# Kernel tuning notes

Measured on AMD Instinct MI355X. Metric: run time of the kernel, lower is better.

The kernel has to match this reference:

```python
import jax, jax.numpy as jnp
import numpy as np

N, E, D_IN, HID, OUT, H = 50000, 800000, 64, 128, 128, 8


def _lin(key, fan_in, fan_out, bias=True):
    k1, k2 = jax.random.split(key)
    W = jax.random.normal(k1, (fan_in, fan_out), jnp.float32) / np.sqrt(fan_in)
    if bias:
        b = jax.random.normal(k2, (fan_out,), jnp.float32) * 0.01
        return W, b
    return (W,)


def setup_inputs() -> dict:
    key = jax.random.key(0)
    ks = jax.random.split(key, 40)
    inp = {
        "x": jax.random.normal(ks[0], (N, D_IN), jnp.float32),
        "edge_index": jax.random.randint(ks[1], (2, E), 0, N, jnp.int64),
        "edge_attr": jax.random.normal(ks[2], (E, D_IN), jnp.float32),
    }
    dims = [(D_IN, HID), (HID, HID), (HID, OUT)]  # (in, heads*out_ch) per layer
    ki = 3
    for l, (di, do) in enumerate(dims):
        inp[f"Wq{l}"], inp[f"bq{l}"] = _lin(ks[ki], di, do); ki += 1
        inp[f"Wk{l}"], inp[f"bk{l}"] = _lin(ks[ki], di, do); ki += 1
        inp[f"Wv{l}"], inp[f"bv{l}"] = _lin(ks[ki], di, do); ki += 1
        (inp[f"We{l}"],) = _lin(ks[ki], D_IN, do, bias=False); ki += 1
        inp[f"Ws{l}"], inp[f"bs{l}"] = _lin(ks[ki], di, do); ki += 1
    for l in range(2):
        inp[f"g{l}"] = jnp.ones((HID,), jnp.float32)
        inp[f"be{l}"] = jnp.zeros((HID,), jnp.float32)
    return inp


def _transformer_conv(x, src, dst, edge_attr, Wq, bq, Wk, bk, Wv, bv, We, Ws, bs):
    n = x.shape[0]
    hc = Wq.shape[1]
    c = hc // H
    q = (x @ Wq + bq).reshape(n, H, c)
    k = (x @ Wk + bk).reshape(n, H, c)
    v = (x @ Wv + bv).reshape(n, H, c)
    e = (edge_attr @ We).reshape(-1, H, c)  # [E,H,c]
    ke = k[src] + e                          # edge-wise key + edge proj
    alpha = jnp.einsum("ehc,ehc->eh", q[dst], ke) / jnp.sqrt(jnp.float32(c))
    m = jax.ops.segment_max(alpha, dst, num_segments=n)
    m = jnp.where(jnp.isfinite(m), m, 0.0)
    p = jnp.exp(alpha - m[dst])
    s = jax.ops.segment_sum(p, dst, num_segments=n)
    a = p / (s[dst] + 1e-16)                 # segment softmax over in-edges
    msg = (v[src] + e) * a[..., None]
    out = jax.ops.segment_sum(msg, dst, num_segments=n).reshape(n, hc)
    return out + x @ Ws + bs                 # root/skip connection


def _bn(x, g, b):
    mu = jnp.mean(x, axis=0)
    var = jnp.mean(jnp.square(x - mu), axis=0)
    return g * (x - mu) * jax.lax.rsqrt(var + 1e-5) + b


def reference(x, edge_index, edge_attr,
              Wq0, bq0, Wk0, bk0, Wv0, bv0, We0, Ws0, bs0,
              Wq1, bq1, Wk1, bk1, Wv1, bv1, We1, Ws1, bs1,
              Wq2, bq2, Wk2, bk2, Wv2, bv2, We2, Ws2, bs2,
              g0, be0, g1, be1):
    src, dst = edge_index[0], edge_index[1]
    h = _transformer_conv(x, src, dst, edge_attr, Wq0, bq0, Wk0, bk0, Wv0, bv0, We0, Ws0, bs0)
    h = jax.nn.relu(_bn(h, g0, be0))
    h = _transformer_conv(h, src, dst, edge_attr, Wq1, bq1, Wk1, bk1, Wv1, bv1, We1, Ws1, bs1)
    h = jax.nn.relu(_bn(h, g1, be1))
    h = _transformer_conv(h, src, dst, edge_attr, Wq2, bq2, Wk2, bk2, Wv2, bv2, We2, Ws2, bs2)
    return h, edge_attr
```

## Files before the change

### kernel.cpp

```cpp
#include <hip/hip_runtime.h>
#include <hip/hip_bf16.h>

typedef __attribute__((ext_vector_type(8))) short short8;
typedef __attribute__((ext_vector_type(4))) float f32x4;
typedef unsigned short ushort_t;
typedef __attribute__((ext_vector_type(2))) unsigned short ushort2v;
typedef __attribute__((ext_vector_type(2))) unsigned int uint2v;
typedef __attribute__((ext_vector_type(4))) unsigned int uint4v;

static __device__ __forceinline__ ushort_t f2bf(float x) {
    __hip_bfloat16 h = __float2bfloat16(x);
    return *(ushort_t*)&h;
}
static __device__ __forceinline__ float bflo(unsigned int u) { return __uint_as_float(u << 16); }
static __device__ __forceinline__ float bfhi(unsigned int u) { return __uint_as_float(u & 0xffff0000u); }
static __device__ __forceinline__ float bfu(ushort_t u) { return __uint_as_float((unsigned int)u << 16); }

template <int CTRL>
static __device__ __forceinline__ float dpp_xadd(float x) {
    int y = __builtin_amdgcn_update_dpp(0, __float_as_int(x), CTRL, 0xF, 0xF, true);
    return x + __int_as_float(y);
}
static __device__ __forceinline__ float swz4_add(float x) {
    int y = __builtin_amdgcn_ds_swizzle(__float_as_int(x), 0x101F);
    return x + __int_as_float(y);
}


__global__ void hist_kernel(const int* __restrict__ dst, int E, int* __restrict__ hist) {
    int i = blockIdx.x * blockDim.x + threadIdx.x;
    if (i < E) atomicAdd(&hist[dst[i]], 1);
}

__global__ __launch_bounds__(1024) void scan_block_kernel(
    const int* __restrict__ hist, int n, int* __restrict__ row_ptr, int* __restrict__ bsums)
{
    __shared__ int lds[1024];
    int tid = threadIdx.x;
    int i = blockIdx.x * 1024 + tid;
    int vv = (i < n) ? hist[i] : 0;
    lds[tid] = vv;
    __syncthreads();
    for (int off = 1; off < 1024; off <<= 1) {
        int t = (tid >= off) ? lds[tid - off] : 0;
        __syncthreads();
        lds[tid] += t;
        __syncthreads();
    }
    if (i < n) row_ptr[i] = lds[tid] - vv;
    if (tid == 1023) bsums[blockIdx.x] = lds[1023];
}

__global__ void scan_tops_kernel(int* __restrict__ bsums, int nb) {
    if (threadIdx.x == 0 && blockIdx.x == 0) {
        int run = 0;
        for (int i = 0; i < nb; i++) { int t = bsums[i]; bsums[i] = run; run += t; }
    }
}

__global__ __launch_bounds__(256) void scan_add_kernel(
    const int* __restrict__ bsums, int n, int total,
    int* __restrict__ row_ptr, int* __restrict__ cursor)
{
    int i = blockIdx.x * blockDim.x + threadIdx.x;
    if (i < n) {
        int vv = row_ptr[i] + bsums[i >> 10];
        row_ptr[i] = vv;
        cursor[i] = vv;
    }
    if (i == 0) row_ptr[n] = total;
}

__global__ void scatter_kernel(const int* __restrict__ src, const int* __restrict__ dst, int E,
                               int* __restrict__ cursor, int* __restrict__ inv, int* __restrict__ srcs) {
    int i = blockIdx.x * blockDim.x + threadIdx.x;
    if (i < E) {
        int d = dst[i];
        int pos = atomicAdd(&cursor[d], 1);
        inv[i] = pos;
        srcs[pos] = src[i];
    }
}

__global__ __launch_bounds__(256) void copy_permute_kernel(
    const float* __restrict__ edge_attr, const int* __restrict__ inv, int E,
    float* __restrict__ out_pass, ushort_t* __restrict__ ea)
{
    int idx = blockIdx.x * blockDim.x + threadIdx.x;
    if (idx >= E * 8) return;
    int i = idx >> 3, seg = idx & 7;
    const float* s = edge_attr + (size_t)i * 64 + seg * 8;
    float4 f0 = *(const float4*)s;
    float4 f1 = *(const float4*)(s + 4);
    float* d = out_pass + (size_t)i * 64 + seg * 8;
    *(float4*)d = f0;
    *(float4*)(d + 4) = f1;
    short8 o;
    o[0] = f2bf(f0.x); o[1] = f2bf(f0.y); o[2] = f2bf(f0.z); o[3] = f2bf(f0.w);
    o[4] = f2bf(f1.x); o[5] = f2bf(f1.y); o[6] = f2bf(f1.z); o[7] = f2bf(f1.w);
    int pos = inv[i];
    *(short8*)(ea + (size_t)pos * 64 + seg * 8) = o;
}

struct PackArgs {
    const float* We[3];
    const float* Wn[3][4];
    const float* bb[3][4];
};

__global__ __launch_bounds__(256) void pack_all_kernel(
    PackArgs pa, ushort_t* __restrict__ BpackE, ushort_t* __restrict__ BpackN,
    float* __restrict__ biasc)
{
    int idx = blockIdx.x * blockDim.x + threadIdx.x;
    if (idx < 24576) {
        int j = idx & 7, lane = (idx >> 3) & 63, kk = (idx >> 9) & 1,
            t = (idx >> 10) & 7, layer = idx >> 13;
        int kdim = kk * 32 + (lane >> 4) * 8 + j;
        int ncol = t * 16 + (lane & 15);
        BpackE[idx] = f2bf(pa.We[layer][kdim * 128 + ncol]);
    } else if (idx < 188416) {
        int local = idx - 24576;
        int layer, DI;
        if (local < 32768) { layer = 0; DI = 64; }
        else if (local < 98304) { layer = 1; DI = 128; local -= 32768; }
        else { layer = 2; DI = 128; local -= 98304; }
        int NKF = DI >> 5;
        int j = local & 7, lane = (local >> 3) & 63;
        int rest = local >> 9;
        int kf = rest % NKF, t = rest / NKF;
        int kdim = kf * 32 + (lane >> 4) * 8 + j;
        int ncol = t * 16 + (lane & 15);
        BpackN[layer * 65536 + local] = f2bf(pa.Wn[layer][ncol >> 7][kdim * 128 + (ncol & 127)]);
    } else if (idx < 189952) {
        int local = idx - 188416;
        int layer = local >> 9, i = local & 511;
        biasc[layer * 512 + i] = pa.bb[layer][i >> 7][i & 127];
    }
}

template <int DI, bool BN>
__global__ __launch_bounds__(256) void node_gemm_mfma_kernel(
    const float* __restrict__ hin, int N,
    const ushort_t* __restrict__ Bpack, const float* __restrict__ biasc,
    const float* __restrict__ scale, const float* __restrict__ shift,
    float* __restrict__ qout, unsigned int* __restrict__ kvout,
    float* __restrict__ skipout)
{
    constexpr int NKF = DI / 32;
    __shared__ float ctile[64][132];
    __shared__ ushort_t ctileK[64][136];
    int wave = threadIdx.x >> 6;
    int lane = threadIdx.x & 63;
    int tid = threadIdx.x;
    int base = blockIdx.x * 64;
    int m0 = base + wave * 16;

    int mrow = min(m0 + (lane & 15), N - 1);
    const float* arow = hin + (size_t)mrow * DI;
    int koff = (lane >> 4) * 8;

    short8 a[NKF];
#pragma unroll
    for (int kf = 0; kf < NKF; kf++) {
        float4 fa = *(const float4*)(arow + kf * 32 + koff);
        float4 fb = *(const float4*)(arow + kf * 32 + koff + 4);
        if constexpr (BN) {
            int c0 = kf * 32 + koff;
            float4 sa = *(const float4*)(scale + c0);
            float4 sb = *(const float4*)(scale + c0 + 4);
            float4 ha = *(const float4*)(shift + c0);
            float4 hb = *(const float4*)(shift + c0 + 4);
            fa.x = fmaxf(fa.x * sa.x + ha.x, 0.f);
            fa.y = fmaxf(fa.y * sa.y + ha.y, 0.f);
            fa.z = fmaxf(fa.z * sa.z + ha.z, 0.f);
            fa.w = fmaxf(fa.w * sa.w + ha.w, 0.f);
            fb.x = fmaxf(fb.x * sb.x + hb.x, 0.f);
            fb.y = fmaxf(fb.y * sb.y + hb.y, 0.f);
            fb.z = fmaxf(fb.z * sb.z + hb.z, 0.f);
            fb.w = fmaxf(fb.w * sb.w + hb.w, 0.f);
        }
        short8 t;
        t[0] = f2bf(fa.x); t[1] = f2bf(fa.y); t[2] = f2bf(fa.z); t[3] = f2bf(fa.w);
        t[4] = f2bf(fb.x); t[5] = f2bf(fb.y); t[6] = f2bf(fb.z); t[7] = f2bf(fb.w);
        a[kf] = t;
    }

    const short8* Bp = (const short8*)Bpack;
    f32x4 acc[32];
#pragma unroll
    for (int t = 0; t < 32; t++) acc[t] = (f32x4){0.f, 0.f, 0.f, 0.f};
#pragma unroll
    for (int t = 0; t < 32; t++) {
#pragma unroll
        for (int kf = 0; kf < NKF; kf++)
            acc[t] = __builtin_amdgcn_mfma_f32_16x16x32_bf16(a[kf], Bp[(t * NKF + kf) * 64 + lane], acc[t], 0, 0, 0);
    }

    int crow = (lane >> 4) * 4;
    int ccol = lane & 15;

#pragma unroll
    for (int t8 = 0; t8 < 8; t8++) {
        float bb = biasc[t8 * 16 + ccol];
#pragma unroll
        for (int r = 0; r < 4; r++)
            ctile[wave * 16 + crow + r][t8 * 16 + ccol] = acc[t8][r] + bb;
    }
    __syncthreads();
#pragma unroll
    for (int it = 0; it < 8; it++) {
        int idx4 = it * 256 + tid;
        int row = idx4 >> 5;
        int c4 = idx4 & 31;
        int gr = base + row;
        if (gr < N)
            *(float4*)(qout + (size_t)gr * 128 + c4 * 4) = *(const float4*)&ctile[row][c4 * 4];
    }
    __syncthreads();

#pragma unroll
    for (int t8 = 0; t8 < 8; t8++) {
        float bb = biasc[128 + t8 * 16 + ccol];
#pragma unroll
        for (int r = 0; r < 4; r++)
            ctileK[wave * 16 + crow + r][t8 * 16 + ccol] = f2bf(acc[8 + t8][r] + bb);
    }
#pragma unroll
    for (int t8 = 0; t8 < 8; t8++) {
        float bb = biasc[256 + t8 * 16 + ccol];
#pragma unroll
        for (int r = 0; r < 4; r++)
            ctile[wave * 16 + crow + r][t8 * 16 + ccol] = acc[16 + t8][r] + bb;
    }
    __syncthreads();
#pragma unroll
    for (int it = 0; it < 4; it++) {
        int idx8 = it * 256 + tid;
        int row = idx8 >> 4;
        int c8 = idx8 & 15;
        int gr = base + row;
        if (gr < N) {
            const float* vs = &ctile[row][c8 * 8];
            uint4v o0, o1;
#pragma unroll
            for (int i = 0; i < 4; i++) {
                ushort2v kp2 = *(const ushort2v*)&ctileK[row][c8 * 8 + 2 * i];
                unsigned int kp = (unsigned int)kp2[0] | ((unsigned int)kp2[1] << 16);
                unsigned int vp = (unsigned int)f2bf(vs[2 * i]) | ((unsigned int)f2bf(vs[2 * i + 1]) << 16);
                if (i < 2) { o0[2 * i] = kp; o0[2 * i + 1] = vp; }
                else       { o1[2 * (i - 2)] = kp; o1[2 * (i - 2) + 1] = vp; }
            }
            unsigned int* dp = kvout + (size_t)gr * 128 + c8 * 8;
            *(uint4v*)dp = o0;
            *(uint4v*)(dp + 4) = o1;
        }
    }
    __syncthreads();

#pragma unroll
    for (int t8 = 0; t8 < 8; t8++) {
        float bb = biasc[384 + t8 * 16 + ccol];
#pragma unroll
        for (int r = 0; r < 4; r++)
            ctile[wave * 16 + crow + r][t8 * 16 + ccol] = acc[24 + t8][r] + bb;
    }
    __syncthreads();
#pragma unroll
    for (int it = 0; it < 8; it++) {
        int idx4 = it * 256 + tid;
        int row = idx4 >> 5;
        int c4 = idx4 & 31;
        int gr = base + row;
        if (gr < N)
            *(float4*)(skipout + (size_t)gr * 128 + c4 * 4) = *(const float4*)&ctile[row][c4 * 4];
    }
}

#define PROCESS8(B)                                                              \
    {                                                                            \
        ushort2v eev[8];                                                         \
        float p[8];                                                              \
        _Pragma("unroll")                                                        \
        for (int u = 0; u < 8; u++)                                              \
            eev[u] = *(const ushort2v*)&elds[wave][(B) * 8 + u][2 * lane];       \
        _Pragma("unroll")                                                        \
        for (int u = 0; u < 8; u++) {                                            \
            uint2v kvp = kvr[(B) * 8 + u];                                       \
            p[u] = qq.x * (bflo(kvp[0]) + bfu(eev[u][0]))                        \
                 + qq.y * (bfhi(kvp[0]) + bfu(eev[u][1]));                       \
        }                                                                        \
        _Pragma("unroll")                                                        \
        for (int u = 0; u < 8; u++) {                                            \
            p[u] = dpp_xadd<0xB1>(p[u]);                                         \
            p[u] = dpp_xadd<0x4E>(p[u]);                                         \
            p[u] = swz4_add(p[u]);                                               \
        }                                                                        \
        _Pragma("unroll")                                                        \
        for (int u = 0; u < 8; u++) {                                            \
            float wv = __expf(p[u]);                                             \
            if (c0 + (B) * 8 + u >= je) wv = 0.f;                                \
            uint2v kvp = kvr[(B) * 8 + u];                                       \
            acc0 += wv * (bflo(kvp[1]) + bfu(eev[u][0]));                        \
            acc1 += wv * (bfhi(kvp[1]) + bfu(eev[u][1]));                        \
            sw += wv;                                                            \
        }                                                                        \
    }

__global__ __launch_bounds__(512) void agg_fused_kernel(
    const int* __restrict__ row_ptr, const int* __restrict__ srcs,
    const float* __restrict__ q, const unsigned int* __restrict__ kvbuf,
    const ushort_t* __restrict__ ea, const ushort_t* __restrict__ BpackWe,
    float* __restrict__ hout, int N)
{
    __shared__ ushort_t bsh[8192];
    __shared__ ushort_t elds[8][16][136];
    int tid = threadIdx.x;
    {
        const short8* s8 = (const short8*)BpackWe;
        short8* d8 = (short8*)bsh;
        d8[tid] = s8[tid];
        d8[512 + tid] = s8[512 + tid];
    }
    __syncthreads();

    int wave = tid >> 6, lane = tid & 63;
    int n = blockIdx.x * 8 + wave;
    if (n >= N) return;

    const float2* q2 = (const float2*)q;
    float2* h2 = (float2*)hout;
    const short8* bs8 = (const short8*)bsh;

    int ch = lane & 15, kg = lane >> 4;
    float2 qq = q2[(size_t)n * 64 + lane];
    qq.x *= 0.25f; qq.y *= 0.25f;
    float2 sk = h2[(size_t)n * 64 + lane];
    float acc0 = 0.f, acc1 = 0.f, sw = 0.f;
    int jb = row_ptr[n], je = row_ptr[n + 1];

    short8 a0 = {}, a1 = {};
    int sv = 0;
    if (jb < je) {
        int j0 = min(jb + ch, je - 1);
        sv = srcs[j0];
        const ushort_t* row0 = ea + (size_t)j0 * 64;
        a0 = *(const short8*)(row0 + kg * 8);
        a1 = *(const short8*)(row0 + 32 + kg * 8);
    }

    for (int c0 = jb; c0 < je; c0 += 16) {
        uint2v kvr[16];
#pragma unroll
        for (int u = 0; u < 16; u++) {
            int su = __builtin_amdgcn_readlane(sv, u);
            kvr[u] = *(const uint2v*)(kvbuf + (size_t)su * 128 + 2 * lane);
        }

#pragma unroll
        for (int t = 0; t < 8; t++) {
            f32x4 z = (f32x4){0.f, 0.f, 0.f, 0.f};
            z = __builtin_amdgcn_mfma_f32_16x16x32_bf16(a0, bs8[(t * 2 + 0) * 64 + lane], z, 0, 0, 0);
            z = __builtin_amdgcn_mfma_f32_16x16x32_bf16(a1, bs8[(t * 2 + 1) * 64 + lane], z, 0, 0, 0);
#pragma unroll
            for (int r = 0; r < 4; r++)
                elds[wave][kg * 4 + r][t * 16 + ch] = f2bf(z[r]);
        }

        int cn = c0 + 16;
        short8 na0 = a0, na1 = a1;
        int nsv = sv;
        if (cn < je) {
            int jn = min(cn + ch, je - 1);
            nsv = srcs[jn];
            const ushort_t* nrow = ea + (size_t)jn * 64;
            na0 = *(const short8*)(nrow + kg * 8);
            na1 = *(const short8*)(nrow + 32 + kg * 8);
        }

        asm volatile("" ::: "memory");

        PROCESS8(0)
        if (c0 + 8 < je) PROCESS8(1)

        a0 = na0; a1 = na1; sv = nsv;
    }
    float inv = 1.0f / (sw + 1e-16f);
    float2 o;
    o.x = acc0 * inv + sk.x;
    o.y = acc1 * inv + sk.y;
    h2[(size_t)n * 64 + lane] = o;
}

__global__ __launch_bounds__(128) void bn_stats_kernel(const float* __restrict__ h, int N,
                                                       float* __restrict__ sums) {
    int f = threadIdx.x;
    float s = 0.f, s2 = 0.f;
    for (int n = blockIdx.x; n < N; n += gridDim.x) {
        float x = h[(size_t)n * 128 + f];
        s += x;
        s2 += x * x;
    }
    atomicAdd(&sums[f], s);
    atomicAdd(&sums[128 + f], s2);
}

__global__ __launch_bounds__(128) void bn_finalize_kernel(
    const float* __restrict__ sums, const float* __restrict__ g,
    const float* __restrict__ be, int N,
    float* __restrict__ scale, float* __restrict__ shift)
{
    int f = threadIdx.x;
    float invN = 1.0f / (float)N;
    float mu = sums[f] * invN;
    float var = sums[128 + f] * invN - mu * mu;
    float sc = g[f] * rsqrtf(var + 1e-5f);
    scale[f] = sc;
    shift[f] = be[f] - mu * sc;
}

extern "C" void kernel_launch(void* const* d_in, const int* in_sizes, int n_in,
                              void* d_out, int out_size, void* d_ws, size_t ws_size,
                              hipStream_t stream)
{
    const float* x = (const float*)d_in[0];
    const int* edge_index = (const int*)d_in[1];
    const float* edge_attr = (const float*)d_in[2];
    int N = in_sizes[0] / 64;
    int E = in_sizes[1] / 2;
    const int* src = edge_index;
    const int* dst = edge_index + E;

    const float* W[3][9];
    for (int l = 0; l < 3; l++)
        for (int i = 0; i < 9; i++) W[l][i] = (const float*)d_in[3 + l * 9 + i];
    const float* g0 = (const float*)d_in[30];
    const float* be0 = (const float*)d_in[31];
    const float* g1 = (const float*)d_in[32];
    const float* be1 = (const float*)d_in[33];

    char* p = (char*)d_ws;
    auto alloc = [&](size_t bytes) -> char* {
        char* r = p;
        p += (bytes + 255) & ~(size_t)255;
        return r;
    };
    float* q = (float*)alloc((size_t)N * 128 * 4);
    unsigned int* kvbuf = (unsigned int*)alloc((size_t)N * 512);
    float* B = (float*)alloc((size_t)N * 128 * 4);
    ushort_t* ea = (ushort_t*)alloc((size_t)E * 64 * 2);
    int* row_ptr = (int*)alloc((size_t)(N + 1) * 4);
    int* cursor = (int*)alloc((size_t)N * 4);
    int* histb = (int*)alloc((size_t)N * 4);
    int* inv = (int*)alloc((size_t)E * 4);
    int* srcs = (int*)alloc((size_t)E * 4);
    int* bsums = (int*)alloc(64 * 4);
    float* sums = (float*)alloc(512 * 4);
    float* bnp = (float*)alloc(512 * 4);
    ushort_t* BpackE = (ushort_t*)alloc((size_t)3 * 8192 * 2);
    ushort_t* BpackN = (ushort_t*)alloc((size_t)3 * 65536 * 2);
    float* biasc = (float*)alloc((size_t)3 * 512 * 4);

    int nb = (N + 1023) / 1024;

    hipMemsetAsync(histb, 0, (size_t)N * 4, stream);
    hipMemsetAsync(sums, 0, 512 * 4, stream);
    hist_kernel<<<(E + 255) / 256, 256, 0, stream>>>(dst, E, histb);
    scan_block_kernel<<<nb, 1024, 0, stream>>>(histb, N, row_ptr, bsums);
    scan_tops_kernel<<<1, 64, 0, stream>>>(bsums, nb);
    scan_add_kernel<<<(N + 255) / 256, 256, 0, stream>>>(bsums, N, E, row_ptr, cursor);
    scatter_kernel<<<(E + 255) / 256, 256, 0, stream>>>(src, dst, E, cursor, inv, srcs);
    copy_permute_kernel<<<(E * 8 + 255) / 256, 256, 0, stream>>>(
        edge_attr, inv, E, (float*)d_out + (size_t)N * 128, ea);

    {
        PackArgs pa;
        for (int l = 0; l < 3; l++) {
            pa.We[l] = W[l][6];
            pa.Wn[l][0] = W[l][0]; pa.Wn[l][1] = W[l][2];
            pa.Wn[l][2] = W[l][4]; pa.Wn[l][3] = W[l][7];
            pa.bb[l][0] = W[l][1]; pa.bb[l][1] = W[l][3];
            pa.bb[l][2] = W[l][5]; pa.bb[l][3] = W[l][8];
        }
        pack_all_kernel<<<(189952 + 255) / 256, 256, 0, stream>>>(pa, BpackE, BpackN, biasc);
    }

    for (int l = 0; l < 3; l++) {
        float* skipbuf = (l == 2) ? (float*)d_out : B;
        if (l == 0)
            node_gemm_mfma_kernel<64, false><<<(N + 63) / 64, 256, 0, stream>>>(
                x, N, BpackN, biasc, nullptr, nullptr, q, kvbuf, skipbuf);
        else
            node_gemm_mfma_kernel<128, true><<<(N + 63) / 64, 256, 0, stream>>>(
                B, N, BpackN + (size_t)l * 65536, biasc + (size_t)l * 512,
                bnp + (size_t)(l - 1) * 256, bnp + (size_t)(l - 1) * 256 + 128,
                q, kvbuf, skipbuf);
        agg_fused_kernel<<<(N + 7) / 8, 512, 0, stream>>>(
            row_ptr, srcs, q, kvbuf, ea, BpackE + (size_t)l * 8192, skipbuf, N);
        if (l < 2) {
            bn_stats_kernel<<<512, 128, 0, stream>>>(skipbuf, N, sums + (size_t)l * 256);
            const float* gg = (l == 0) ? g0 : g1;
            const float* bb = (l == 0) ? be0 : be1;
            bn_finalize_kernel<<<1, 128, 0, stream>>>(
                sums + (size_t)l * 256, gg, bb, N,
                bnp + (size_t)l * 256, bnp + (size_t)l * 256 + 128);
        }
    }
}
```

Measured before the change: 662.2 us.

## Bucket nodes by in-degree so aggregation waves in a block share similar work

Adds a counting-sort pass over node in-degrees (histogram, scan, scatter) that builds a node permutation, and the fused aggregation kernel now processes nodes in that order. Each block of 8 waves then holds nodes of similar degree, which is meant to reduce load imbalance and tail effects inside blocks. In exchange it adds three small kernels plus a memset, and the atomic scatter makes node order within a degree bucket nondeterministic. Node accesses to q, skip and output rows also become scattered rather than sequential, which may hurt locality.

```diff
diff --git a/kernel.cpp b/kernel.cpp
--- a/kernel.cpp
+++ b/kernel.cpp
@@ -79,6 +79,45 @@
         int pos = atomicAdd(&cursor[d], 1);
         inv[i] = pos;
         srcs[pos] = src[i];
+    }
+}
+
+__global__ __launch_bounds__(256) void deg_hist_kernel(
+    const int* __restrict__ row_ptr, int N, int* __restrict__ dhist)
+{
+    int i = blockIdx.x * blockDim.x + threadIdx.x;
+    if (i < N) {
+        int d = min(row_ptr[i + 1] - row_ptr[i], 255);
+        atomicAdd(&dhist[d], 1);
+    }
+}
+
+__global__ __launch_bounds__(256) void deg_scan_kernel(
+    const int* __restrict__ dhist, int* __restrict__ dcur)
+{
+    __shared__ int lds[256];
+    int tid = threadIdx.x;
+    int vv = dhist[tid];
+    lds[tid] = vv;
+    __syncthreads();
+    for (int off = 1; off < 256; off <<= 1) {
+        int t = (tid >= off) ? lds[tid - off] : 0;
+        __syncthreads();
+        lds[tid] += t;
+        __syncthreads();
+    }
+    dcur[tid] = lds[tid] - vv;
+}
+
+__global__ __launch_bounds__(256) void deg_scatter_kernel(
+    const int* __restrict__ row_ptr, int N, int* __restrict__ dcur,
+    int* __restrict__ nodeperm)
+{
+    int i = blockIdx.x * blockDim.x + threadIdx.x;
+    if (i < N) {
+        int d = min(row_ptr[i + 1] - row_ptr[i], 255);
+        int pos = atomicAdd(&dcur[d], 1);
+        nodeperm[pos] = i;
     }
 }
 
@@ -309,6 +348,7 @@
 
 __global__ __launch_bounds__(512) void agg_fused_kernel(
     const int* __restrict__ row_ptr, const int* __restrict__ srcs,
+    const int* __restrict__ nodeperm,
     const float* __restrict__ q, const unsigned int* __restrict__ kvbuf,
     const ushort_t* __restrict__ ea, const ushort_t* __restrict__ BpackWe,
     float* __restrict__ hout, int N)
@@ -325,8 +365,9 @@
     __syncthreads();
 
     int wave = tid >> 6, lane = tid & 63;
-    int n = blockIdx.x * 8 + wave;
-    if (n >= N) return;
+    int slot = blockIdx.x * 8 + wave;
+    if (slot >= N) return;
+    int n = nodeperm[slot];
 
     const float2* q2 = (const float2*)q;
     float2* h2 = (float2*)hout;
@@ -454,7 +495,10 @@
     int* histb = (int*)alloc((size_t)N * 4);
     int* inv = (int*)alloc((size_t)E * 4);
     int* srcs = (int*)alloc((size_t)E * 4);
+    int* nodeperm = (int*)alloc((size_t)N * 4);
     int* bsums = (int*)alloc(64 * 4);
+    int* dhist = (int*)alloc(256 * 4);
+    int* dcur = (int*)alloc(256 * 4);
     float* sums = (float*)alloc(512 * 4);
     float* bnp = (float*)alloc(512 * 4);
     ushort_t* BpackE = (ushort_t*)alloc((size_t)3 * 8192 * 2);
@@ -465,6 +509,7 @@
 
     hipMemsetAsync(histb, 0, (size_t)N * 4, stream);
     hipMemsetAsync(sums, 0, 512 * 4, stream);
+    hipMemsetAsync(dhist, 0, 256 * 4, stream);
     hist_kernel<<<(E + 255) / 256, 256, 0, stream>>>(dst, E, histb);
     scan_block_kernel<<<nb, 1024, 0, stream>>>(histb, N, row_ptr, bsums);
     scan_tops_kernel<<<1, 64, 0, stream>>>(bsums, nb);
@@ -472,6 +517,9 @@
     scatter_kernel<<<(E + 255) / 256, 256, 0, stream>>>(src, dst, E, cursor, inv, srcs);
     copy_permute_kernel<<<(E * 8 + 255) / 256, 256, 0, stream>>>(
         edge_attr, inv, E, (float*)d_out + (size_t)N * 128, ea);
+    deg_hist_kernel<<<(N + 255) / 256, 256, 0, stream>>>(row_ptr, N, dhist);
+    deg_scan_kernel<<<1, 256, 0, stream>>>(dhist, dcur);
+    deg_scatter_kernel<<<(N + 255) / 256, 256, 0, stream>>>(row_ptr, N, dcur, nodeperm);
 
     {
         PackArgs pa;
@@ -496,7 +544,7 @@
                 bnp + (size_t)(l - 1) * 256, bnp + (size_t)(l - 1) * 256 + 128,
                 q, kvbuf, skipbuf);
         agg_fused_kernel<<<(N + 7) / 8, 512, 0, stream>>>(
-            row_ptr, srcs, q, kvbuf, ea, BpackE + (size_t)l * 8192, skipbuf, N);
+            row_ptr, srcs, nodeperm, q, kvbuf, ea, BpackE + (size_t)l * 8192, skipbuf, N);
         if (l < 2) {
             bn_stats_kernel<<<512, 128, 0, stream>>>(skipbuf, N, sums + (size_t)l * 256);
             const float* gg = (l == 0) ? g0 : g1;
```

Measured after the change: 932.5 us. +40.8%, slower.
